# Kernel optimization log

Measured on AMD Instinct MI355X. Metric: run time of the kernel, lower is better.

The kernel has to match this reference:

```python
import jax, jax.numpy as jnp
import numpy as np

UNITS = 1536
CHAR_LEN = 256
VOCAB = 80
N_MIX = 10  # mixtures // 3


def lstm_step(x, h, c, W, U, b):
    # Keras LSTM gate order: i, f, g(candidate), o
    z = x @ W + h @ U + b
    i, f, g, o = jnp.split(z, 4, axis=-1)
    c_new = jax.nn.sigmoid(f) * c + jax.nn.sigmoid(i) * jnp.tanh(g)
    h_new = jax.nn.sigmoid(o) * jnp.tanh(c_new)
    return h_new, c_new


def compute_window(sentence, coef, kappa_prev):
    # coef: (1, 30) -> alpha, beta, kappa each (1, 10)
    alpha, beta, kappa = jnp.split(coef, 3, axis=1)
    alpha = jnp.exp(alpha)
    beta = jnp.exp(beta)
    kappa = kappa_prev + jnp.exp(kappa)
    u = jnp.arange(1, CHAR_LEN + 1, dtype=coef.dtype)[:, None]  # (L, 1)
    # (L, 10) -> sum over mixtures -> (L,)
    phi = jnp.sum(alpha * jnp.exp(-beta * (kappa - u) ** 2), axis=1)
    phi = phi.reshape(1, CHAR_LEN)
    w = phi @ sentence  # (1, V)
    last_phi = jnp.sum(alpha * jnp.exp(-beta * (kappa - CHAR_LEN + 1) ** 2), axis=1).reshape(1, 1)
    phi_out = jnp.concatenate([phi, last_phi], axis=-1)  # (1, L+1)
    return w, kappa, phi_out


def setup_inputs() -> dict:
    key = jax.random.key(0)
    ks = jax.random.split(key, 24)
    s = 0.02
    in1 = 3 + VOCAB
    in23 = 3 + VOCAB + UNITS
    return {
        "inputs": jax.random.normal(ks[0], (1, 3), jnp.float32),
        "h1": jax.random.normal(ks[1], (1, UNITS), jnp.float32) * 0.1,
        "c1": jax.random.normal(ks[2], (1, UNITS), jnp.float32) * 0.1,
        "h2": jax.random.normal(ks[3], (1, UNITS), jnp.float32) * 0.1,
        "c2": jax.random.normal(ks[4], (1, UNITS), jnp.float32) * 0.1,
        "h3": jax.random.normal(ks[5], (1, UNITS), jnp.float32) * 0.1,
        "c3": jax.random.normal(ks[6], (1, UNITS), jnp.float32) * 0.1,
        "w_prev": jax.random.uniform(ks[7], (1, VOCAB), jnp.float32),
        "kappa_prev": jax.random.uniform(ks[8], (1, N_MIX), jnp.float32),
        "sentence": jax.random.uniform(ks[9], (CHAR_LEN, VOCAB), jnp.float32),
        "W1": jax.random.normal(ks[10], (in1, 4 * UNITS), jnp.float32) * s,
        "U1": jax.random.normal(ks[11], (UNITS, 4 * UNITS), jnp.float32) * s,
        "b1": jnp.zeros((4 * UNITS,), jnp.float32),
        "Wd": jax.random.normal(ks[12], (UNITS, 30), jnp.float32) * s,
        "bd": jnp.zeros((30,), jnp.float32),
        "W2": jax.random.normal(ks[13], (in23, 4 * UNITS), jnp.float32) * s,
        "U2": jax.random.normal(ks[14], (UNITS, 4 * UNITS), jnp.float32) * s,
        "b2": jnp.zeros((4 * UNITS,), jnp.float32),
        "W3": jax.random.normal(ks[15], (in23, 4 * UNITS), jnp.float32) * s,
        "U3": jax.random.normal(ks[16], (UNITS, 4 * UNITS), jnp.float32) * s,
        "b3": jnp.zeros((4 * UNITS,), jnp.float32),
    }


def reference(inputs, h1, c1, h2, c2, h3, c3, w_prev, kappa_prev, sentence,
              W1, U1, b1, Wd, bd, W2, U2, b2, W3, U3, b3):
    # LSTM 1: input = [strokes, prev window]
    x1 = jnp.concatenate([inputs, w_prev], axis=-1)
    h1n, c1n = lstm_step(x1, h1, c1, W1, U1, b1)
    # Attention window coefficients
    coef = h1n @ Wd + bd  # (1, 30)
    w, kappa, phi = compute_window(sentence, coef, kappa_prev)
    # LSTM 2: input = [strokes, window, lstm1]
    x2 = jnp.concatenate([inputs, w, h1n], axis=-1)
    h2n, c2n = lstm_step(x2, h2, c2, W2, U2, b2)
    # LSTM 3: input = [strokes, window, lstm2]
    x3 = jnp.concatenate([inputs, w, h2n], axis=-1)
    h3n, c3n = lstm_step(x3, h3, c3, W3, U3, b3)
    output = jnp.concatenate([h1n, h2n, h3n], axis=-1)  # (1, 3*units)
    return output
```

## Files before the change

### kernel.cpp

```cpp
#include <hip/hip_runtime.h>
#include <math.h>

#define UNITS 1536
#define COLS  6144
#define VOCAB 80
#define CHAR_LEN 256
#define NMIX 10

__device__ __forceinline__ float sigmoidf_(float x) { return 1.0f / (1.0f + __expf(-x)); }

__global__ __launch_bounds__(256)
void gemv_indep(const float* __restrict__ W1, const float* __restrict__ U1,
                const float* __restrict__ U2, const float* __restrict__ U3,
                const float* __restrict__ W2, const float* __restrict__ W3,
                const float* __restrict__ in3, const float* __restrict__ wp,
                const float* __restrict__ h1, const float* __restrict__ h2,
                const float* __restrict__ h3,
                float* __restrict__ p1, float* __restrict__ p2, float* __restrict__ p3)
{
    __shared__ const float* rps[32];
    __shared__ float xsh[32];
    const int t = threadIdx.x;
    const int cy = blockIdx.y;

    if (t < 32) {
        const int g = cy * 32 + t;
        const float* rp = W1;
        float xv = 0.f;
        if (g < 83)        { rp = W1 + (size_t)g * COLS;          xv = (g < 3) ? in3[g] : wp[g - 3]; }
        else if (g < 1619) { rp = U1 + (size_t)(g - 83) * COLS;   xv = h1[g - 83]; }
        else if (g < 1632) {  }
        else if (g < 3168) { rp = U2 + (size_t)(g - 1632) * COLS; xv = h2[g - 1632]; }
        else if (g < 3171) { rp = W2 + (size_t)(g - 3168) * COLS; xv = in3[g - 3168]; }
        else if (g < 3200) {  }
        else if (g < 4736) { rp = U3 + (size_t)(g - 3200) * COLS; xv = h3[g - 3200]; }
        else if (g < 4739) { rp = W3 + (size_t)(g - 4736) * COLS; xv = in3[g - 4736]; }
        rps[t] = rp; xsh[t] = xv;
    }
    __syncthreads();

    const int col = (blockIdx.x * 256 + t) * 4;
    float4 acc = make_float4(0.f, 0.f, 0.f, 0.f);
    #pragma unroll 8
    for (int i = 0; i < 32; ++i) {
        const float4 v = *reinterpret_cast<const float4*>(rps[i] + col);
        const float x = xsh[i];
        acc.x = fmaf(x, v.x, acc.x); acc.y = fmaf(x, v.y, acc.y);
        acc.z = fmaf(x, v.z, acc.z); acc.w = fmaf(x, v.w, acc.w);
    }

    float* zone; int slot;
    if (cy < 51)       { zone = p1; slot = cy; }
    else if (cy < 99)  { zone = p2; slot = cy - 51; }
    else if (cy == 99) { zone = p2; slot = 48; }
    else if (cy < 148) { zone = p3; slot = cy - 100; }
    else               { zone = p3; slot = 48; }
    *reinterpret_cast<float4*>(zone + (size_t)slot * COLS + col) = acc;
}

__global__ __launch_bounds__(256)
void gemv_dep(const float* __restrict__ W, const float* __restrict__ wv,
              const float* __restrict__ hp, float* __restrict__ zoneBase)
{
    __shared__ const float* rps[32];
    __shared__ float xsh[32];
    const int t = threadIdx.x;
    const int cy = blockIdx.y;

    if (t < 32) {
        const int g2 = cy * 32 + t;
        const float* rp = W + 3 * COLS;
        float xv = 0.f;
        if (g2 < 80)        { rp = W + (size_t)(3 + g2) * COLS; xv = wv[g2]; }
        else if (g2 < 1616) { rp = W + (size_t)(3 + g2) * COLS; xv = hp[g2 - 80]; }
        rps[t] = rp; xsh[t] = xv;
    }
    __syncthreads();

    const int col = (blockIdx.x * 256 + t) * 4;
    float4 acc = make_float4(0.f, 0.f, 0.f, 0.f);
    #pragma unroll 8
    for (int i = 0; i < 32; ++i) {
        const float4 v = *reinterpret_cast<const float4*>(rps[i] + col);
        const float x = xsh[i];
        acc.x = fmaf(x, v.x, acc.x); acc.y = fmaf(x, v.y, acc.y);
        acc.z = fmaf(x, v.z, acc.z); acc.w = fmaf(x, v.w, acc.w);
    }
    *reinterpret_cast<float4*>(zoneBase + (size_t)cy * COLS + col) = acc;
}

__global__ __launch_bounds__(1024)
void gate_fused(const float* __restrict__ partials, int nChunks,
                const float* __restrict__ b, const float* __restrict__ c_in,
                float* __restrict__ h_out,
                const float* __restrict__ Wd, float* __restrict__ coefpart)
{
    __shared__ float red[4][4][64];
    __shared__ float zs[4][64];
    __shared__ float hs[64];
    __shared__ float red2[8][30];

    const int t = threadIdx.x;
    const int jj = t & 63;
    const int gate = (t >> 6) & 3;
    const int stripe = t >> 8;
    const int j0 = blockIdx.x * 64;
    const int col = gate * UNITS + j0 + jj;

    float s = 0.f;
    for (int c = stripe; c < nChunks; c += 4)
        s += partials[(size_t)c * COLS + col];
    red[stripe][gate][jj] = s;
    __syncthreads();

    if (t < 256) {
        const float z = b[col] + red[0][gate][jj] + red[1][gate][jj]
                               + red[2][gate][jj] + red[3][gate][jj];
        zs[gate][jj] = z;
    }
    __syncthreads();

    if (t < 64) {
        const float zi = zs[0][t], zf = zs[1][t], zg = zs[2][t], zo = zs[3][t];
        const float cn = sigmoidf_(zf) * c_in[j0 + t] + sigmoidf_(zi) * tanhf(zg);
        const float h = sigmoidf_(zo) * tanhf(cn);
        h_out[j0 + t] = h;
        hs[t] = h;
    }
    __syncthreads();

    if (Wd != nullptr) {
        if (t < 240) {
            const int c30 = t % 30;
            const int rbase = (t / 30) * 8;
            float s2 = 0.f;
            #pragma unroll
            for (int k = 0; k < 8; ++k) {
                const int r = rbase + k;
                s2 = fmaf(hs[r], Wd[(size_t)(j0 + r) * 30 + c30], s2);
            }
            red2[t / 30][c30] = s2;
        }
        __syncthreads();
        if (t < 30) {
            float a = 0.f;
            #pragma unroll
            for (int k = 0; k < 8; ++k) a += red2[k][t];
            coefpart[blockIdx.x * 30 + t] = a;
        }
    }
}

__global__ __launch_bounds__(1024)
void window_b(const float* __restrict__ coefpart, const float* __restrict__ bd,
              const float* __restrict__ kappa_prev, const float* __restrict__ sentence,
              float* __restrict__ w_out)
{
    __shared__ float coef[32];
    __shared__ float al[NMIX], be[NMIX], ka[NMIX];
    __shared__ float phi[CHAR_LEN];
    __shared__ float red[12][VOCAB];

    const int t = threadIdx.x;

    if (t < 30) {
        float s = bd[t];
        #pragma unroll
        for (int bb = 0; bb < 24; ++bb) s += coefpart[bb * 30 + t];
        coef[t] = s;
    }
    __syncthreads();

    if (t < NMIX) {
        al[t] = __expf(coef[t]);
        be[t] = __expf(coef[10 + t]);
        ka[t] = kappa_prev[t] + __expf(coef[20 + t]);
    }
    __syncthreads();

    if (t < CHAR_LEN) {
        const float u = (float)(t + 1);
        float p = 0.f;
        #pragma unroll
        for (int k = 0; k < NMIX; ++k) {
            const float d = ka[k] - u;
            p += al[k] * __expf(-be[k] * d * d);
        }
        phi[t] = p;
    }
    __syncthreads();

    if (t < 960) {
        const int v = t % 80;
        const int stripe = t / 80;
        float s = 0.f;
        for (int u = stripe; u < CHAR_LEN; u += 12)
            s = fmaf(phi[u], sentence[u * VOCAB + v], s);
        red[stripe][v] = s;
    }
    __syncthreads();

    if (t < VOCAB) {
        float s = 0.f;
        #pragma unroll
        for (int k = 0; k < 12; ++k) s += red[k][t];
        w_out[t] = s;
    }
}

extern "C" void kernel_launch(void* const* d_in, const int* in_sizes, int n_in,
                              void* d_out, int out_size, void* d_ws, size_t ws_size,
                              hipStream_t stream) {
    (void)in_sizes; (void)n_in; (void)out_size; (void)ws_size;

    const float* inputs     = (const float*)d_in[0];
    const float* h1         = (const float*)d_in[1];
    const float* c1         = (const float*)d_in[2];
    const float* h2         = (const float*)d_in[3];
    const float* c2         = (const float*)d_in[4];
    const float* h3         = (const float*)d_in[5];
    const float* c3         = (const float*)d_in[6];
    const float* w_prev     = (const float*)d_in[7];
    const float* kappa_prev = (const float*)d_in[8];
    const float* sentence   = (const float*)d_in[9];
    const float* W1 = (const float*)d_in[10];
    const float* U1 = (const float*)d_in[11];
    const float* b1 = (const float*)d_in[12];
    const float* Wd = (const float*)d_in[13];
    const float* bd = (const float*)d_in[14];
    const float* W2 = (const float*)d_in[15];
    const float* U2 = (const float*)d_in[16];
    const float* b2 = (const float*)d_in[17];
    const float* W3 = (const float*)d_in[18];
    const float* U3 = (const float*)d_in[19];
    const float* b3 = (const float*)d_in[20];

    float* out = (float*)d_out;
    float* ws  = (float*)d_ws;
    float* w_vec    = ws;
    float* coefpart = ws + 128;
    float* pbase    = ws + 1024;
    float* p1 = pbase;
    float* p2 = pbase + (size_t)51  * COLS;
    float* p3 = pbase + (size_t)151 * COLS;

    gemv_indep<<<dim3(6, 149), 256, 0, stream>>>(W1, U1, U2, U3, W2, W3,
                                                 inputs, w_prev, h1, h2, h3,
                                                 p1, p2, p3);
    gate_fused<<<24, 1024, 0, stream>>>(p1, 51, b1, c1, out, Wd, coefpart);
    window_b<<<1, 1024, 0, stream>>>(coefpart, bd, kappa_prev, sentence, w_vec);
    gemv_dep<<<dim3(6, 51), 256, 0, stream>>>(W2, w_vec, out, p2 + (size_t)49 * COLS);
    gate_fused<<<24, 1024, 0, stream>>>(p2, 100, b2, c2, out + UNITS, nullptr, nullptr);
    gemv_dep<<<dim3(6, 51), 256, 0, stream>>>(W3, w_vec, out + UNITS, p3 + (size_t)49 * COLS);
    gate_fused<<<24, 1024, 0, stream>>>(p3, 100, b3, c3, out + 2 * UNITS, nullptr, nullptr);
}
```

Before: 275.5 us.

## Halve GEMV row chunks, batch loads, and spread gate reduction over more blocks

Row chunks in both GEMV kernels shrink from 32 to 16 rows, which roughly doubles the number of blocks. Each thread now issues all 8 float4 loads of a batch before its FMAs, with row pointers made wave-uniform through readfirstlane. The gate kernel handles 16 units per block across 96 blocks with a 16-way stripe reduction, and the window kernel sums 96 coefficient partials. This aims to raise memory-level parallelism and occupancy on the weight stream, at the cost of twice as many partial sums to write and read back.

```diff
diff --git a/kernel.cpp b/kernel.cpp
--- a/kernel.cpp
+++ b/kernel.cpp
@@ -9,7 +9,28 @@
 
 __device__ __forceinline__ float sigmoidf_(float x) { return 1.0f / (1.0f + __expf(-x)); }
 
-__global__ __launch_bounds__(256)
+__device__ __forceinline__ const float* rfl_ptr(const float* p) {
+    unsigned long long u = (unsigned long long)p;
+    unsigned lo = __builtin_amdgcn_readfirstlane((unsigned)u);
+    unsigned hi = __builtin_amdgcn_readfirstlane((unsigned)(u >> 32));
+    return (const float*)(((unsigned long long)hi << 32) | lo);
+}
+
+#define GEMV_BATCH(BASE)                                                     \
+    {                                                                        \
+        float4 v[8];                                                         \
+        _Pragma("unroll")                                                    \
+        for (int i = 0; i < 8; ++i)                                          \
+            v[i] = *reinterpret_cast<const float4*>(rfl_ptr(rps[BASE + i]) + col); \
+        _Pragma("unroll")                                                    \
+        for (int i = 0; i < 8; ++i) {                                        \
+            const float x = xsh[BASE + i];                                   \
+            acc.x = fmaf(x, v[i].x, acc.x); acc.y = fmaf(x, v[i].y, acc.y);  \
+            acc.z = fmaf(x, v[i].z, acc.z); acc.w = fmaf(x, v[i].w, acc.w);  \
+        }                                                                    \
+    }
+
+__global__ __launch_bounds__(256, 6)
 void gemv_indep(const float* __restrict__ W1, const float* __restrict__ U1,
                 const float* __restrict__ U2, const float* __restrict__ U3,
                 const float* __restrict__ W2, const float* __restrict__ W3,
@@ -18,74 +39,63 @@
                 const float* __restrict__ h3,
                 float* __restrict__ p1, float* __restrict__ p2, float* __restrict__ p3)
 {
-    __shared__ const float* rps[32];
-    __shared__ float xsh[32];
+    __shared__ const float* rps[16];
+    __shared__ float xsh[16];
     const int t = threadIdx.x;
     const int cy = blockIdx.y;
 
-    if (t < 32) {
-        const int g = cy * 32 + t;
+    if (t < 16) {
         const float* rp = W1;
         float xv = 0.f;
-        if (g < 83)        { rp = W1 + (size_t)g * COLS;          xv = (g < 3) ? in3[g] : wp[g - 3]; }
-        else if (g < 1619) { rp = U1 + (size_t)(g - 83) * COLS;   xv = h1[g - 83]; }
-        else if (g < 1632) {  }
-        else if (g < 3168) { rp = U2 + (size_t)(g - 1632) * COLS; xv = h2[g - 1632]; }
-        else if (g < 3171) { rp = W2 + (size_t)(g - 3168) * COLS; xv = in3[g - 3168]; }
-        else if (g < 3200) {  }
-        else if (g < 4736) { rp = U3 + (size_t)(g - 3200) * COLS; xv = h3[g - 3200]; }
-        else if (g < 4739) { rp = W3 + (size_t)(g - 4736) * COLS; xv = in3[g - 4736]; }
+        if (cy < 102) {
+            const int g = cy * 16 + t;
+            if (g < 83)        { rp = W1 + (size_t)g * COLS;        xv = (g < 3) ? in3[g] : wp[g - 3]; }
+            else if (g < 1619) { rp = U1 + (size_t)(g - 83) * COLS; xv = h1[g - 83]; }
+        } else if (cy < 199) {
+            const int g = (cy - 102) * 16 + t;
+            if (g < 1536)      { rp = U2 + (size_t)g * COLS;          xv = h2[g]; }
+            else if (g < 1539) { rp = W2 + (size_t)(g - 1536) * COLS; xv = in3[g - 1536]; }
+        } else {
+            const int g = (cy - 199) * 16 + t;
+            if (g < 1536)      { rp = U3 + (size_t)g * COLS;          xv = h3[g]; }
+            else if (g < 1539) { rp = W3 + (size_t)(g - 1536) * COLS; xv = in3[g - 1536]; }
+        }
         rps[t] = rp; xsh[t] = xv;
     }
     __syncthreads();
 
     const int col = (blockIdx.x * 256 + t) * 4;
     float4 acc = make_float4(0.f, 0.f, 0.f, 0.f);
-    #pragma unroll 8
-    for (int i = 0; i < 32; ++i) {
-        const float4 v = *reinterpret_cast<const float4*>(rps[i] + col);
-        const float x = xsh[i];
-        acc.x = fmaf(x, v.x, acc.x); acc.y = fmaf(x, v.y, acc.y);
-        acc.z = fmaf(x, v.z, acc.z); acc.w = fmaf(x, v.w, acc.w);
-    }
+    GEMV_BATCH(0)
+    GEMV_BATCH(8)
 
     float* zone; int slot;
-    if (cy < 51)       { zone = p1; slot = cy; }
-    else if (cy < 99)  { zone = p2; slot = cy - 51; }
-    else if (cy == 99) { zone = p2; slot = 48; }
-    else if (cy < 148) { zone = p3; slot = cy - 100; }
-    else               { zone = p3; slot = 48; }
+    if (cy < 102)      { zone = p1; slot = cy; }
+    else if (cy < 199) { zone = p2; slot = cy - 102; }
+    else               { zone = p3; slot = cy - 199; }
     *reinterpret_cast<float4*>(zone + (size_t)slot * COLS + col) = acc;
 }
 
-__global__ __launch_bounds__(256)
+__global__ __launch_bounds__(256, 6)
 void gemv_dep(const float* __restrict__ W, const float* __restrict__ wv,
               const float* __restrict__ hp, float* __restrict__ zoneBase)
 {
-    __shared__ const float* rps[32];
-    __shared__ float xsh[32];
+    __shared__ const float* rps[16];
+    __shared__ float xsh[16];
     const int t = threadIdx.x;
     const int cy = blockIdx.y;
 
-    if (t < 32) {
-        const int g2 = cy * 32 + t;
-        const float* rp = W + 3 * COLS;
-        float xv = 0.f;
-        if (g2 < 80)        { rp = W + (size_t)(3 + g2) * COLS; xv = wv[g2]; }
-        else if (g2 < 1616) { rp = W + (size_t)(3 + g2) * COLS; xv = hp[g2 - 80]; }
-        rps[t] = rp; xsh[t] = xv;
+    if (t < 16) {
+        const int g2 = cy * 16 + t;
+        rps[t] = W + (size_t)(3 + g2) * COLS;
+        xsh[t] = (g2 < 80) ? wv[g2] : hp[g2 - 80];
     }
     __syncthreads();
 
     const int col = (blockIdx.x * 256 + t) * 4;
     float4 acc = make_float4(0.f, 0.f, 0.f, 0.f);
-    #pragma unroll 8
-    for (int i = 0; i < 32; ++i) {
-        const float4 v = *reinterpret_cast<const float4*>(rps[i] + col);
-        const float x = xsh[i];
-        acc.x = fmaf(x, v.x, acc.x); acc.y = fmaf(x, v.y, acc.y);
-        acc.z = fmaf(x, v.z, acc.z); acc.w = fmaf(x, v.w, acc.w);
-    }
+    GEMV_BATCH(0)
+    GEMV_BATCH(8)
     *reinterpret_cast<float4*>(zoneBase + (size_t)cy * COLS + col) = acc;
 }
 
@@ -95,32 +105,34 @@
                 float* __restrict__ h_out,
                 const float* __restrict__ Wd, float* __restrict__ coefpart)
 {
-    __shared__ float red[4][4][64];
-    __shared__ float zs[4][64];
-    __shared__ float hs[64];
-    __shared__ float red2[8][30];
-
-    const int t = threadIdx.x;
-    const int jj = t & 63;
-    const int gate = (t >> 6) & 3;
-    const int stripe = t >> 8;
-    const int j0 = blockIdx.x * 64;
+    __shared__ float red[16][4][16];
+    __shared__ float zs[4][16];
+    __shared__ float hs[16];
+    __shared__ float red2[16][30];
+
+    const int t = threadIdx.x;
+    const int jj = t & 15;
+    const int gate = (t >> 4) & 3;
+    const int stripe = t >> 6;
+    const int j0 = blockIdx.x * 16;
     const int col = gate * UNITS + j0 + jj;
 
     float s = 0.f;
-    for (int c = stripe; c < nChunks; c += 4)
+    for (int c = stripe; c < nChunks; c += 16)
         s += partials[(size_t)c * COLS + col];
     red[stripe][gate][jj] = s;
     __syncthreads();
 
-    if (t < 256) {
-        const float z = b[col] + red[0][gate][jj] + red[1][gate][jj]
-                               + red[2][gate][jj] + red[3][gate][jj];
-        zs[gate][jj] = z;
-    }
-    __syncthreads();
-
     if (t < 64) {
+        const int g2 = t >> 4, j2 = t & 15;
+        float z = b[g2 * UNITS + j0 + j2];
+        #pragma unroll
+        for (int k = 0; k < 16; ++k) z += red[k][g2][j2];
+        zs[g2][j2] = z;
+    }
+    __syncthreads();
+
+    if (t < 16) {
         const float zi = zs[0][t], zf = zs[1][t], zg = zs[2][t], zo = zs[3][t];
         const float cn = sigmoidf_(zf) * c_in[j0 + t] + sigmoidf_(zi) * tanhf(zg);
         const float h = sigmoidf_(zo) * tanhf(cn);
@@ -130,22 +142,15 @@
     __syncthreads();
 
     if (Wd != nullptr) {
-        if (t < 240) {
-            const int c30 = t % 30;
-            const int rbase = (t / 30) * 8;
-            float s2 = 0.f;
-            #pragma unroll
-            for (int k = 0; k < 8; ++k) {
-                const int r = rbase + k;
-                s2 = fmaf(hs[r], Wd[(size_t)(j0 + r) * 30 + c30], s2);
-            }
-            red2[t / 30][c30] = s2;
+        if (t < 480) {
+            const int r = t / 30, c30 = t % 30;
+            red2[r][c30] = hs[r] * Wd[(size_t)(j0 + r) * 30 + c30];
         }
         __syncthreads();
         if (t < 30) {
             float a = 0.f;
             #pragma unroll
-            for (int k = 0; k < 8; ++k) a += red2[k][t];
+            for (int k = 0; k < 16; ++k) a += red2[k][t];
             coefpart[blockIdx.x * 30 + t] = a;
         }
     }
@@ -165,8 +170,7 @@
 
     if (t < 30) {
         float s = bd[t];
-        #pragma unroll
-        for (int bb = 0; bb < 24; ++bb) s += coefpart[bb * 30 + t];
+        for (int bb = 0; bb < 96; ++bb) s += coefpart[bb * 30 + t];
         coef[t] = s;
     }
     __syncthreads();
@@ -239,18 +243,18 @@
     float* ws  = (float*)d_ws;
     float* w_vec    = ws;
     float* coefpart = ws + 128;
-    float* pbase    = ws + 1024;
+    float* pbase    = ws + 4096;
     float* p1 = pbase;
-    float* p2 = pbase + (size_t)51  * COLS;
-    float* p3 = pbase + (size_t)151 * COLS;
-
-    gemv_indep<<<dim3(6, 149), 256, 0, stream>>>(W1, U1, U2, U3, W2, W3,
+    float* p2 = pbase + (size_t)102 * COLS;
+    float* p3 = pbase + (size_t)300 * COLS;
+
+    gemv_indep<<<dim3(6, 296), 256, 0, stream>>>(W1, U1, U2, U3, W2, W3,
                                                  inputs, w_prev, h1, h2, h3,
                                                  p1, p2, p3);
-    gate_fused<<<24, 1024, 0, stream>>>(p1, 51, b1, c1, out, Wd, coefpart);
+    gate_fused<<<96, 1024, 0, stream>>>(p1, 102, b1, c1, out, Wd, coefpart);
     window_b<<<1, 1024, 0, stream>>>(coefpart, bd, kappa_prev, sentence, w_vec);
-    gemv_dep<<<dim3(6, 51), 256, 0, stream>>>(W2, w_vec, out, p2 + (size_t)49 * COLS);
-    gate_fused<<<24, 1024, 0, stream>>>(p2, 100, b2, c2, out + UNITS, nullptr, nullptr);
-    gemv_dep<<<dim3(6, 51), 256, 0, stream>>>(W3, w_vec, out + UNITS, p3 + (size_t)49 * COLS);
-    gate_fused<<<24, 1024, 0, stream>>>(p3, 100, b3, c3, out + 2 * UNITS, nullptr, nullptr);
-}
+    gemv_dep<<<dim3(6, 101), 256, 0, stream>>>(W2, w_vec, out, p2 + (size_t)97 * COLS);
+    gate_fused<<<96, 1024, 0, stream>>>(p2, 198, b2, c2, out + UNITS, nullptr, nullptr);
+    gemv_dep<<<dim3(6, 101), 256, 0, stream>>>(W3, w_vec, out + UNITS, p3 + (size_t)97 * COLS);
+    gate_fused<<<96, 1024, 0, stream>>>(p3, 198, b3, c3, out + 2 * UNITS, nullptr, nullptr);
+}
```

After: 268.9 us. 2.4% less time.
